# Kernel optimization log

Measured on AMD Instinct MI355X. Metric: run time of the kernel, lower is better.

The kernel has to match this reference:

```python
import jax, jax.numpy as jnp
import numpy as np

MAX_JOINTS = 143

def setup_inputs() -> dict:
    key = jax.random.key(0)
    ks = jax.random.split(key, 8)
    d_model, latent_dim, feat = 256, 512, 13
    s = lambda n: 1.0 / np.sqrt(n)
    return {
        "z": jax.random.normal(ks[0], (32, latent_dim), jnp.float32),
        "W_latent": jax.random.normal(ks[1], (latent_dim, d_model), jnp.float32) * s(latent_dim),
        "b_latent": jnp.zeros((d_model,), jnp.float32),
        "joint_emb": jax.random.normal(ks[2], (MAX_JOINTS, d_model), jnp.float32),
        "frame_emb": jax.random.normal(ks[3], (120, d_model), jnp.float32),
        "ln_gamma": jnp.ones((d_model,), jnp.float32),
        "ln_beta": jnp.zeros((d_model,), jnp.float32),
        "W1": jax.random.normal(ks[4], (d_model, d_model), jnp.float32) * s(d_model),
        "b1": jnp.zeros((d_model,), jnp.float32),
        "W2": jax.random.normal(ks[5], (d_model, feat), jnp.float32) * s(d_model),
        "b2": jnp.zeros((feat,), jnp.float32),
        "max_frames": 120,
    }

def reference(z, W_latent, b_latent, joint_emb, frame_emb, ln_gamma, ln_beta, W1, b1, W2, b2, max_frames):
    # base: [B, d]
    base = z @ W_latent + b_latent
    fe = frame_emb[:max_frames]  # [F, d]
    # three-way broadcast sum -> [B, J, F, d]
    hidden = base[:, None, None, :] + joint_emb[None, :, None, :] + fe[None, None, :, :]
    # LayerNorm over last dim (eps=1e-5, torch default)
    mu = jnp.mean(hidden, axis=-1, keepdims=True)
    var = jnp.mean(jnp.square(hidden - mu), axis=-1, keepdims=True)
    h = (hidden - mu) * jax.lax.rsqrt(var + 1e-5) * ln_gamma + ln_beta
    # MLP: Linear -> exact GELU -> Linear
    h = jax.nn.gelu(h @ W1 + b1, approximate=False)
    out = h @ W2 + b2  # [B, J, F, feat]
    return jnp.transpose(out, (0, 1, 3, 2))  # [B, J, feat, F]
```

## Files before the change

kernel.cpp:

```cpp
#include <hip/hip_runtime.h>
#include <hip/hip_bf16.h>
#include <hip/hip_cooperative_groups.h>

namespace cg = cooperative_groups;

typedef __bf16 bf16x8 __attribute__((ext_vector_type(8)));
typedef float  f32x4  __attribute__((ext_vector_type(4)));
typedef float  f32x2  __attribute__((ext_vector_type(2)));

#define B_  32
#define J_  143
#define F_  120
#define D_  256
#define L_  512
#define C_  13
#define M_  4576
#define MP_ 4736
#define FE0 4576
#define NK  512
#define NN  384
#define GRID_  763
#define PAIRS_ 2288

static __device__ __forceinline__ unsigned short bits(__bf16 h) {
  return __builtin_bit_cast(unsigned short, h);
}

__device__ __forceinline__ f32x2 gelu2(f32x2 u) {
  f32x2 x2 = u * u;
  f32x2 t  = u * (x2 * -0.1029432f + -2.3022082f);
  f32x2 e;
  e.x = __builtin_amdgcn_exp2f(t.x);
  e.y = __builtin_amdgcn_exp2f(t.y);
  f32x2 d = e + 1.0f;
  f32x2 r;
  r.x = __builtin_amdgcn_rcpf(d.x);
  r.y = __builtin_amdgcn_rcpf(d.y);
  return u * r;
}

__global__ __launch_bounds__(256, 3) void fused_kernel(
    int phase,
    const float* __restrict__ z, const float* __restrict__ Wl,
    const float* __restrict__ bl, const float* __restrict__ joint,
    const float* __restrict__ fe, const float* __restrict__ gamma,
    const float* __restrict__ beta, const float* __restrict__ W1,
    const float* __restrict__ b1, const float* __restrict__ W2,
    const float* __restrict__ b2,
    float* __restrict__ base, unsigned short* __restrict__ BT,
    float* __restrict__ bW1, float* __restrict__ Sfe, float* __restrict__ Sfe2,
    unsigned short* __restrict__ W2T, float* __restrict__ zerov,
    float* __restrict__ PX, float* __restrict__ Sc, float* __restrict__ Sc2,
    float* __restrict__ out) {
  __shared__ float zs[L_];
  __shared__ float ra[4], rb[4];
  __shared__ float pc[2][256], bw[256], rstdl[2][128];
  __shared__ __align__(16) unsigned short w2l[4096];

  const int tid  = threadIdx.x;
  const int lane = tid & 63, wv = tid >> 6;
  const int lrow = lane & 15, lgrp = lane >> 4;
  const int bid  = blockIdx.x;
  const bool coop = (phase == 0);

  if (coop || phase == 1) {
    if (bid < 32) {
      zs[tid]       = z[bid * L_ + tid];
      zs[tid + 256] = z[bid * L_ + tid + 256];
      __syncthreads();
      float acc = 0.f;
      #pragma unroll 32
      for (int k = 0; k < L_; ++k) acc = __builtin_fmaf(zs[k], Wl[k * D_ + tid], acc);
      base[bid * D_ + tid] = acc + bl[tid];
    } else if (bid < 433) {
      const int n = bid - 32;
      if (n < 256) {
        const float w1v = W1[tid * D_ + n];
        float a = gamma[tid] * w1v;
        float b = beta[tid] * w1v;
        const float wg = a;
        #pragma unroll
        for (int m = 1; m < 64; m <<= 1) { a += __shfl_xor(a, m); b += __shfl_xor(b, m); }
        if (lane == 0) { ra[wv] = a; rb[wv] = b; }
        __syncthreads();
        const float cs = ra[0] + ra[1] + ra[2] + ra[3];
        if (tid == 0) bW1[n] = rb[0] + rb[1] + rb[2] + rb[3] + b1[n];
        const float m = __builtin_fmaf(cs, -1.f / 256.f, wg);
        const __bf16 hi = (__bf16)m;
        const __bf16 lo = (__bf16)(m - (float)hi);
        BT[n * NK + tid]       = bits(hi);
        BT[n * NK + 256 + tid] = bits(lo);
      } else if (n < 376) {
        const int f = n - 256;
        const float v = fe[f * D_ + tid];
        float a = v, b = v * v;
        #pragma unroll
        for (int m = 1; m < 64; m <<= 1) { a += __shfl_xor(a, m); b += __shfl_xor(b, m); }
        if (lane == 0) { ra[wv] = a; rb[wv] = b; }
        __syncthreads();
        if (tid == 0) {
          Sfe[f]  = ra[0] + ra[1] + ra[2] + ra[3];
          Sfe2[f] = rb[0] + rb[1] + rb[2] + rb[3];
        }
        const __bf16 hi = (__bf16)v;
        const __bf16 lo = (__bf16)(v - (float)hi);
        BT[n * NK + tid]       = bits(hi);
        BT[n * NK + 256 + tid] = bits(lo);
      } else if (n < 384) {
        BT[n * NK + tid] = 0; BT[n * NK + 256 + tid] = 0;
      } else if (n < 400) {
        const int c = n - 384;
        const float v = (c < C_) ? W2[tid * C_ + c] : 0.f;
        W2T[c * D_ + tid] = bits((__bf16)v);
      } else {
        zerov[tid] = 0.f;
      }
    }
  }
  if (coop) cg::this_grid().sync();

  if ((coop || phase == 2) && bid < 444) {
    const int rb_ = bid / 6, cb_ = bid % 6;
    const int rowbase = rb_ * 64 + wv * 16;
    const int colbase = cb_ * 64;
    const int r = rowbase + lrow;

    const float *p1, *p2;
    if (r < M_) {
      const int b = r / J_, j = r - b * J_;
      p1 = base + b * D_; p2 = joint + j * D_;
    } else if (r < FE0 + F_) {
      p1 = fe + (r - FE0) * D_; p2 = zerov;
    } else {
      p1 = zerov; p2 = zerov;
    }

    const unsigned short* Bp = BT + (size_t)(colbase + lrow) * NK + lgrp * 8;
    f32x4 acc[4] = {};
    float ssum = 0.f, ssq = 0.f;
    #pragma unroll
    for (int s8 = 0; s8 < 8; ++s8) {
      const int k0 = s8 * 32 + lgrp * 8;
      const float4 ca = *(const float4*)(p1 + k0);
      const float4 cb4 = *(const float4*)(p1 + k0 + 4);
      const float4 da = *(const float4*)(p2 + k0);
      const float4 db = *(const float4*)(p2 + k0 + 4);
      const float c[8] = {ca.x + da.x, ca.y + da.y, ca.z + da.z, ca.w + da.w,
                          cb4.x + db.x, cb4.y + db.y, cb4.z + db.z, cb4.w + db.w};
      bf16x8 ahi, alo;
      #pragma unroll
      for (int e = 0; e < 8; ++e) {
        const __bf16 h = (__bf16)c[e];
        ahi[e] = h;
        alo[e] = (__bf16)(c[e] - (float)h);
      }
      if (cb_ == 0) {
        #pragma unroll
        for (int e = 0; e < 8; ++e) { ssum += c[e]; ssq = __builtin_fmaf(c[e], c[e], ssq); }
      }
      bf16x8 bhi[4], blo[4];
      #pragma unroll
      for (int nf = 0; nf < 4; ++nf) {
        bhi[nf] = *(const bf16x8*)(Bp + (size_t)nf * 16 * NK + s8 * 32);
        blo[nf] = *(const bf16x8*)(Bp + (size_t)nf * 16 * NK + 256 + s8 * 32);
      }
      #pragma unroll
      for (int nf = 0; nf < 4; ++nf)
        acc[nf] = __builtin_amdgcn_mfma_f32_16x16x32_bf16(ahi, bhi[nf], acc[nf], 0, 0, 0);
      #pragma unroll
      for (int nf = 0; nf < 4; ++nf)
        acc[nf] = __builtin_amdgcn_mfma_f32_16x16x32_bf16(alo, bhi[nf], acc[nf], 0, 0, 0);
      #pragma unroll
      for (int nf = 0; nf < 4; ++nf)
        acc[nf] = __builtin_amdgcn_mfma_f32_16x16x32_bf16(ahi, blo[nf], acc[nf], 0, 0, 0);
    }

    if (cb_ == 0) {
      ssum += __shfl_xor(ssum, 16); ssum += __shfl_xor(ssum, 32);
      ssq  += __shfl_xor(ssq, 16);  ssq  += __shfl_xor(ssq, 32);
      if (lgrp == 0) { Sc[r] = ssum; Sc2[r] = ssq; }
    }

    #pragma unroll
    for (int nf = 0; nf < 4; ++nf)
      #pragma unroll
      for (int r4 = 0; r4 < 4; ++r4)
        PX[(size_t)(rowbase + lgrp * 4 + r4) * NN + colbase + nf * 16 + lrow] = acc[nf][r4];
  }
  if (coop) cg::this_grid().sync();

  if (coop || phase == 3) {
    bw[tid] = bW1[tid];
    {
      const int rr = tid >> 4;
      const int b0 = tid * 32;
      const int sb = b0 ^ ((rr & 7) << 4);
      *(uint4*)((char*)w2l + sb)        = *(const uint4*)((const char*)W2T + b0);
      *(uint4*)((char*)w2l + (sb ^ 16)) = *(const uint4*)((const char*)W2T + b0 + 16);
    }
    const float bias = (lrow < C_) ? b2[lrow] : 0.f;

    const int r0 = wv * 32 + lrow, r1 = r0 + 16;
    const int f0 = r0 < F_ ? r0 : F_ - 1;
    const int f1 = r1 < F_ ? r1 : F_ - 1;
    const float* __restrict__ q0p = PX + (size_t)(FE0 + f0) * NN + lgrp * 8;
    const float* __restrict__ q1p = PX + (size_t)(FE0 + f1) * NN + lgrp * 8;

    for (int pair = bid; pair < PAIRS_; pair += (int)gridDim.x) {
      const int bj0 = pair * 2;
      __syncthreads();

      #pragma unroll
      for (int q = 0; q < 2; ++q) pc[q][tid] = PX[(size_t)(bj0 + q) * NN + tid];
      {
        const int q = tid >> 7;
        const int f = tid & 127;
        const int fc = f < F_ ? f : F_ - 1;
        const float X = PX[(size_t)(bj0 + q) * NN + 256 + fc];
        const float mu = (Sc[bj0 + q] + Sfe[fc]) * (1.f / 256.f);
        const float ms = __builtin_fmaf(2.f, X, Sc2[bj0 + q] + Sfe2[fc]) * (1.f / 256.f);
        rstdl[q][f] = rsqrtf(ms - mu * mu + 1e-5f);
      }
      __syncthreads();

      f32x2 RS0[2], RS1[2];
      #pragma unroll
      for (int q = 0; q < 2; ++q) {
        const float a = rstdl[q][r0], b = rstdl[q][r1];
        RS0[q].x = a; RS0[q].y = a;
        RS1[q].x = b; RS1[q].y = b;
      }

      float4 qa0 = *(const float4*)(q0p), qa1 = *(const float4*)(q0p + 4);
      float4 qb0 = *(const float4*)(q1p), qb1 = *(const float4*)(q1p + 4);

      f32x4 acc[2][2] = {};
      #pragma unroll
      for (int s = 0; s < 8; ++s) {
        const int n0 = s * 32 + lgrp * 8;
        float4 na0, na1, nb0, nb1;
        if (s < 7) {
          na0 = *(const float4*)(q0p + (s + 1) * 32);
          na1 = *(const float4*)(q0p + (s + 1) * 32 + 4);
          nb0 = *(const float4*)(q1p + (s + 1) * 32);
          nb1 = *(const float4*)(q1p + (s + 1) * 32 + 4);
        }
        const bf16x8 w2f = *(const bf16x8*)((const char*)w2l +
            ((lrow * 512 + n0 * 2) ^ ((lrow & 7) << 4)));
        const float q0v[8] = {qa0.x, qa0.y, qa0.z, qa0.w, qa1.x, qa1.y, qa1.z, qa1.w};
        const float q1v[8] = {qb0.x, qb0.y, qb0.z, qb0.w, qb1.x, qb1.y, qb1.z, qb1.w};
        bf16x8 af[2][2];
        #pragma unroll
        for (int ep = 0; ep < 4; ++ep) {
          const int e0 = 2 * ep;
          f32x2 Q0, Q1, BV;
          Q0.x = q0v[e0]; Q0.y = q0v[e0 + 1];
          Q1.x = q1v[e0]; Q1.y = q1v[e0 + 1];
          BV = *(const f32x2*)(&bw[n0 + e0]);
          #pragma unroll
          for (int q = 0; q < 2; ++q) {
            const f32x2 P = *(const f32x2*)(&pc[q][n0 + e0]);
            const f32x2 U0 = __builtin_elementwise_fma(RS0[q], P + Q0, BV);
            const f32x2 U1 = __builtin_elementwise_fma(RS1[q], P + Q1, BV);
            const f32x2 G0 = gelu2(U0);
            const f32x2 G1 = gelu2(U1);
            af[q][0][e0] = (__bf16)G0.x; af[q][0][e0 + 1] = (__bf16)G0.y;
            af[q][1][e0] = (__bf16)G1.x; af[q][1][e0 + 1] = (__bf16)G1.y;
          }
        }
        #pragma unroll
        for (int q = 0; q < 2; ++q) {
          acc[q][0] = __builtin_amdgcn_mfma_f32_16x16x32_bf16(af[q][0], w2f, acc[q][0], 0, 0, 0);
          acc[q][1] = __builtin_amdgcn_mfma_f32_16x16x32_bf16(af[q][1], w2f, acc[q][1], 0, 0, 0);
        }
        qa0 = na0; qa1 = na1; qb0 = nb0; qb1 = nb1;
      }

      if (lrow < C_) {
        #pragma unroll
        for (int q = 0; q < 2; ++q)
          #pragma unroll
          for (int mf = 0; mf < 2; ++mf) {
            const int f = wv * 32 + mf * 16 + lgrp * 4;
            if (f < F_) {
              float4 v;
              v.x = acc[q][mf][0] + bias;
              v.y = acc[q][mf][1] + bias;
              v.z = acc[q][mf][2] + bias;
              v.w = acc[q][mf][3] + bias;
              *(float4*)(out + (size_t)(bj0 + q) * (C_ * F_) + lrow * F_ + f) = v;
            }
          }
      }
    }
  }
}

extern "C" void kernel_launch(void* const* d_in, const int* in_sizes, int n_in,
                              void* d_out, int out_size, void* d_ws, size_t ws_size,
                              hipStream_t stream) {
  const float* z     = (const float*)d_in[0];
  const float* Wl    = (const float*)d_in[1];
  const float* bl    = (const float*)d_in[2];
  const float* joint = (const float*)d_in[3];
  const float* fe    = (const float*)d_in[4];
  const float* gamma = (const float*)d_in[5];
  const float* beta  = (const float*)d_in[6];
  const float* W1    = (const float*)d_in[7];
  const float* b1    = (const float*)d_in[8];
  const float* W2    = (const float*)d_in[9];
  const float* b2    = (const float*)d_in[10];
  float* out = (float*)d_out;

  char* ws = (char*)d_ws;
  float*          base  = (float*)(ws + 0);
  unsigned short* W2T   = (unsigned short*)(ws + 32768);
  float*          bW1   = (float*)(ws + 40960);
  float*          Sfe   = (float*)(ws + 41984);
  float*          Sfe2  = (float*)(ws + 42496);
  float*          Sc    = (float*)(ws + 43008);
  float*          Sc2   = (float*)(ws + 61952);
  float*          zerov = (float*)(ws + 80896);
  unsigned short* BT    = (unsigned short*)(ws + 81920);
  float*          PX    = (float*)(ws + 8388608);

  int phase0 = 0;
  void* args[] = {
    (void*)&phase0,
    (void*)&z, (void*)&Wl, (void*)&bl, (void*)&joint, (void*)&fe,
    (void*)&gamma, (void*)&beta, (void*)&W1, (void*)&b1, (void*)&W2, (void*)&b2,
    (void*)&base, (void*)&BT, (void*)&bW1, (void*)&Sfe, (void*)&Sfe2,
    (void*)&W2T, (void*)&zerov, (void*)&PX, (void*)&Sc, (void*)&Sc2, (void*)&out
  };

  int maxB = 0;
  hipError_t qe = hipOccupancyMaxActiveBlocksPerMultiprocessor(&maxB, fused_kernel, 256, 0);
  const bool coopOK = (qe == hipSuccess) && (maxB >= 3);

  if (coopOK) {
    hipLaunchCooperativeKernel((const void*)fused_kernel, dim3(GRID_), dim3(256),
                               args, 0, stream);
  } else {
    fused_kernel<<<433, 256, 0, stream>>>(1, z, Wl, bl, joint, fe, gamma, beta, W1,
        b1, W2, b2, base, BT, bW1, Sfe, Sfe2, W2T, zerov, PX, Sc, Sc2, out);
    fused_kernel<<<444, 256, 0, stream>>>(2, z, Wl, bl, joint, fe, gamma, beta, W1,
        b1, W2, b2, base, BT, bW1, Sfe, Sfe2, W2T, zerov, PX, Sc, Sc2, out);
    fused_kernel<<<PAIRS_, 256, 0, stream>>>(3, z, Wl, bl, joint, fe, gamma, beta, W1,
        b1, W2, b2, base, BT, bW1, Sfe, Sfe2, W2T, zerov, PX, Sc, Sc2, out);
  }
}
```

Before: 83.86 us.

## Split cooperative fused kernel into three ordinary launches with wider phase-3 blocks

Replaces the single cooperative kernel and its two grid-wide barriers with three separate kernels: prep, the split-bf16 GEMM, and the LayerNorm/GELU/second-GEMM stage. The prep stage now handles W1 column reductions in 4 blocks of 64 columns each instead of 256 single-column blocks. The final stage launches one block per 4 (b,j) rows instead of a persistent grid looping over pairs. This removes grid-sync cost and the occupancy constraint, in exchange for two extra launch boundaries and more per-block setup work in the final stage.

```diff
diff --git a/kernel.cpp b/kernel.cpp
--- a/kernel.cpp
+++ b/kernel.cpp
@@ -1,8 +1,5 @@
 #include <hip/hip_runtime.h>
 #include <hip/hip_bf16.h>
-#include <hip/hip_cooperative_groups.h>
-
-namespace cg = cooperative_groups;
 
 typedef __bf16 bf16x8 __attribute__((ext_vector_type(8)));
 typedef float  f32x4  __attribute__((ext_vector_type(4)));
@@ -19,8 +16,6 @@
 #define FE0 4576
 #define NK  512
 #define NN  384
-#define GRID_  763
-#define PAIRS_ 2288
 
 static __device__ __forceinline__ unsigned short bits(__bf16 h) {
   return __builtin_bit_cast(unsigned short, h);
@@ -39,260 +34,279 @@
   return u * r;
 }
 
-__global__ __launch_bounds__(256, 3) void fused_kernel(
-    int phase,
+__global__ __launch_bounds__(256) void prep_kernel(
     const float* __restrict__ z, const float* __restrict__ Wl,
-    const float* __restrict__ bl, const float* __restrict__ joint,
-    const float* __restrict__ fe, const float* __restrict__ gamma,
-    const float* __restrict__ beta, const float* __restrict__ W1,
-    const float* __restrict__ b1, const float* __restrict__ W2,
-    const float* __restrict__ b2,
+    const float* __restrict__ bl, const float* __restrict__ W1,
+    const float* __restrict__ gamma, const float* __restrict__ beta,
+    const float* __restrict__ b1, const float* __restrict__ fe,
+    const float* __restrict__ W2,
     float* __restrict__ base, unsigned short* __restrict__ BT,
     float* __restrict__ bW1, float* __restrict__ Sfe, float* __restrict__ Sfe2,
-    unsigned short* __restrict__ W2T, float* __restrict__ zerov,
-    float* __restrict__ PX, float* __restrict__ Sc, float* __restrict__ Sc2,
-    float* __restrict__ out) {
+    unsigned short* __restrict__ W2T, float* __restrict__ zerov) {
+  const int t = threadIdx.x, bid = blockIdx.x;
+  const int lane = t & 63, wv = t >> 6;
   __shared__ float zs[L_];
   __shared__ float ra[4], rb[4];
-  __shared__ float pc[2][256], bw[256], rstdl[2][128];
+  __shared__ float gml[256], btl[256];
+  __shared__ float redg[4][64], redb[4][64];
+  __shared__ float csl[64];
+
+  if (bid < 32) {
+    zs[t]       = z[bid * L_ + t];
+    zs[t + 256] = z[bid * L_ + t + 256];
+    __syncthreads();
+    float acc = 0.f;
+    #pragma unroll 32
+    for (int k = 0; k < L_; ++k) acc = __builtin_fmaf(zs[k], Wl[k * D_ + t], acc);
+    base[bid * D_ + t] = acc + bl[t];
+    return;
+  }
+  if (bid < 36) {
+    const int n0 = (bid - 32) * 64;
+    const int c  = t & 63;
+    const int kg = t >> 6;
+    gml[t] = gamma[t];
+    btl[t] = beta[t];
+    __syncthreads();
+    float wg = 0.f, wb = 0.f;
+    #pragma unroll 16
+    for (int kk = 0; kk < 64; ++kk) {
+      const int k = kg * 64 + kk;
+      const float w1v = W1[k * D_ + n0 + c];
+      wg = __builtin_fmaf(gml[k], w1v, wg);
+      wb = __builtin_fmaf(btl[k], w1v, wb);
+    }
+    redg[kg][c] = wg;
+    redb[kg][c] = wb;
+    __syncthreads();
+    if (t < 64) {
+      const float cs = redg[0][t] + redg[1][t] + redg[2][t] + redg[3][t];
+      const float bs = redb[0][t] + redb[1][t] + redb[2][t] + redb[3][t];
+      csl[t] = cs * (1.f / 256.f);
+      bW1[n0 + t] = bs + b1[n0 + t];
+    }
+    __syncthreads();
+    const float csc = csl[c];
+    #pragma unroll 16
+    for (int kk = 0; kk < 64; ++kk) {
+      const int k = kg * 64 + kk;
+      const float w1v = W1[k * D_ + n0 + c];
+      const float m = __builtin_fmaf(gml[k], w1v, -csc);
+      const __bf16 hi = (__bf16)m;
+      const __bf16 lo = (__bf16)(m - (float)hi);
+      BT[(n0 + c) * NK + k]       = bits(hi);
+      BT[(n0 + c) * NK + 256 + k] = bits(lo);
+    }
+    return;
+  }
+  if (bid < 156) {
+    const int f = bid - 36;
+    const float v = fe[f * D_ + t];
+    float a = v, b = v * v;
+    #pragma unroll
+    for (int m = 1; m < 64; m <<= 1) { a += __shfl_xor(a, m); b += __shfl_xor(b, m); }
+    if (lane == 0) { ra[wv] = a; rb[wv] = b; }
+    __syncthreads();
+    if (t == 0) {
+      Sfe[f]  = ra[0] + ra[1] + ra[2] + ra[3];
+      Sfe2[f] = rb[0] + rb[1] + rb[2] + rb[3];
+    }
+    const __bf16 hi = (__bf16)v;
+    const __bf16 lo = (__bf16)(v - (float)hi);
+    BT[(256 + f) * NK + t]       = bits(hi);
+    BT[(256 + f) * NK + 256 + t] = bits(lo);
+    return;
+  }
+  #pragma unroll
+  for (int i = 0; i < 16; ++i)
+    BT[376 * NK + i * 256 + t] = 0;
+  #pragma unroll
+  for (int c = 0; c < 16; ++c) {
+    const float v = (c < C_) ? W2[t * C_ + c] : 0.f;
+    W2T[c * D_ + t] = bits((__bf16)v);
+  }
+  zerov[t] = 0.f;
+}
+
+__global__ __launch_bounds__(256, 4) void gemmB_kernel(
+    const float* __restrict__ base, const float* __restrict__ joint,
+    const float* __restrict__ fe, const float* __restrict__ zerov,
+    const unsigned short* __restrict__ BT,
+    float* __restrict__ PX, float* __restrict__ Sc, float* __restrict__ Sc2) {
+  const int tid = threadIdx.x, lane = tid & 63, wave = tid >> 6;
+  const int lrow = lane & 15, lgrp = lane >> 4;
+  const int rb_ = blockIdx.x / 6, cb_ = blockIdx.x % 6;
+  const int rowbase = rb_ * 64 + wave * 16;
+  const int colbase = cb_ * 64;
+  const int r = rowbase + lrow;
+
+  const float *p1, *p2;
+  if (r < M_) {
+    const int b = r / J_, j = r - b * J_;
+    p1 = base + b * D_; p2 = joint + j * D_;
+  } else if (r < FE0 + F_) {
+    p1 = fe + (r - FE0) * D_; p2 = zerov;
+  } else {
+    p1 = zerov; p2 = zerov;
+  }
+
+  const unsigned short* Bp = BT + (size_t)(colbase + lrow) * NK + lgrp * 8;
+  f32x4 acc[4] = {};
+  float ssum = 0.f, ssq = 0.f;
+  #pragma unroll
+  for (int s8 = 0; s8 < 8; ++s8) {
+    const int k0 = s8 * 32 + lgrp * 8;
+    const float4 ca = *(const float4*)(p1 + k0);
+    const float4 cb4 = *(const float4*)(p1 + k0 + 4);
+    const float4 da = *(const float4*)(p2 + k0);
+    const float4 db = *(const float4*)(p2 + k0 + 4);
+    const float c[8] = {ca.x + da.x, ca.y + da.y, ca.z + da.z, ca.w + da.w,
+                        cb4.x + db.x, cb4.y + db.y, cb4.z + db.z, cb4.w + db.w};
+    bf16x8 ahi, alo;
+    #pragma unroll
+    for (int e = 0; e < 8; ++e) {
+      const __bf16 h = (__bf16)c[e];
+      ahi[e] = h;
+      alo[e] = (__bf16)(c[e] - (float)h);
+    }
+    if (cb_ == 0) {
+      #pragma unroll
+      for (int e = 0; e < 8; ++e) { ssum += c[e]; ssq = __builtin_fmaf(c[e], c[e], ssq); }
+    }
+    bf16x8 bhi[4], blo[4];
+    #pragma unroll
+    for (int nf = 0; nf < 4; ++nf) {
+      bhi[nf] = *(const bf16x8*)(Bp + (size_t)nf * 16 * NK + s8 * 32);
+      blo[nf] = *(const bf16x8*)(Bp + (size_t)nf * 16 * NK + 256 + s8 * 32);
+    }
+    #pragma unroll
+    for (int nf = 0; nf < 4; ++nf)
+      acc[nf] = __builtin_amdgcn_mfma_f32_16x16x32_bf16(ahi, bhi[nf], acc[nf], 0, 0, 0);
+    #pragma unroll
+    for (int nf = 0; nf < 4; ++nf)
+      acc[nf] = __builtin_amdgcn_mfma_f32_16x16x32_bf16(alo, bhi[nf], acc[nf], 0, 0, 0);
+    #pragma unroll
+    for (int nf = 0; nf < 4; ++nf)
+      acc[nf] = __builtin_amdgcn_mfma_f32_16x16x32_bf16(ahi, blo[nf], acc[nf], 0, 0, 0);
+  }
+
+  if (cb_ == 0) {
+    ssum += __shfl_xor(ssum, 16); ssum += __shfl_xor(ssum, 32);
+    ssq  += __shfl_xor(ssq, 16);  ssq  += __shfl_xor(ssq, 32);
+    if (lgrp == 0) { Sc[r] = ssum; Sc2[r] = ssq; }
+  }
+
+  #pragma unroll
+  for (int nf = 0; nf < 4; ++nf)
+    #pragma unroll
+    for (int r4 = 0; r4 < 4; ++r4)
+      PX[(size_t)(rowbase + lgrp * 4 + r4) * NN + colbase + nf * 16 + lrow] = acc[nf][r4];
+}
+
+__global__ __launch_bounds__(256, 4) void mainC_kernel(
+    const float* __restrict__ PX, const float* __restrict__ bW1,
+    const float* __restrict__ Sc, const float* __restrict__ Sc2,
+    const float* __restrict__ Sfe, const float* __restrict__ Sfe2,
+    const unsigned short* __restrict__ W2T, const float* __restrict__ b2,
+    float* __restrict__ out) {
+  __shared__ float pc[4][256], bw[256], rstdl[4][128];
   __shared__ __align__(16) unsigned short w2l[4096];
-
-  const int tid  = threadIdx.x;
-  const int lane = tid & 63, wv = tid >> 6;
+  const int tid = threadIdx.x, lane = tid & 63, wv = tid >> 6;
   const int lrow = lane & 15, lgrp = lane >> 4;
-  const int bid  = blockIdx.x;
-  const bool coop = (phase == 0);
-
-  if (coop || phase == 1) {
-    if (bid < 32) {
-      zs[tid]       = z[bid * L_ + tid];
-      zs[tid + 256] = z[bid * L_ + tid + 256];
-      __syncthreads();
-      float acc = 0.f;
-      #pragma unroll 32
-      for (int k = 0; k < L_; ++k) acc = __builtin_fmaf(zs[k], Wl[k * D_ + tid], acc);
-      base[bid * D_ + tid] = acc + bl[tid];
-    } else if (bid < 433) {
-      const int n = bid - 32;
-      if (n < 256) {
-        const float w1v = W1[tid * D_ + n];
-        float a = gamma[tid] * w1v;
-        float b = beta[tid] * w1v;
-        const float wg = a;
-        #pragma unroll
-        for (int m = 1; m < 64; m <<= 1) { a += __shfl_xor(a, m); b += __shfl_xor(b, m); }
-        if (lane == 0) { ra[wv] = a; rb[wv] = b; }
-        __syncthreads();
-        const float cs = ra[0] + ra[1] + ra[2] + ra[3];
-        if (tid == 0) bW1[n] = rb[0] + rb[1] + rb[2] + rb[3] + b1[n];
-        const float m = __builtin_fmaf(cs, -1.f / 256.f, wg);
-        const __bf16 hi = (__bf16)m;
-        const __bf16 lo = (__bf16)(m - (float)hi);
-        BT[n * NK + tid]       = bits(hi);
-        BT[n * NK + 256 + tid] = bits(lo);
-      } else if (n < 376) {
-        const int f = n - 256;
-        const float v = fe[f * D_ + tid];
-        float a = v, b = v * v;
-        #pragma unroll
-        for (int m = 1; m < 64; m <<= 1) { a += __shfl_xor(a, m); b += __shfl_xor(b, m); }
-        if (lane == 0) { ra[wv] = a; rb[wv] = b; }
-        __syncthreads();
-        if (tid == 0) {
-          Sfe[f]  = ra[0] + ra[1] + ra[2] + ra[3];
-          Sfe2[f] = rb[0] + rb[1] + rb[2] + rb[3];
+  const int bj0 = blockIdx.x * 4;
+
+  #pragma unroll
+  for (int q = 0; q < 4; ++q) pc[q][tid] = PX[(size_t)(bj0 + q) * NN + tid];
+  bw[tid] = bW1[tid];
+  {
+    const int rr = tid >> 4;
+    const int b0 = tid * 32;
+    const int sb = b0 ^ ((rr & 7) << 4);
+    *(uint4*)((char*)w2l + sb)        = *(const uint4*)((const char*)W2T + b0);
+    *(uint4*)((char*)w2l + (sb ^ 16)) = *(const uint4*)((const char*)W2T + b0 + 16);
+  }
+  #pragma unroll
+  for (int qq = 0; qq < 2; ++qq) {
+    const int idx = tid + qq * 256;
+    const int q = idx >> 7;
+    const int f = idx & 127;
+    const int fc = f < F_ ? f : F_ - 1;
+    const float X = PX[(size_t)(bj0 + q) * NN + 256 + fc];
+    const float mu = (Sc[bj0 + q] + Sfe[fc]) * (1.f / 256.f);
+    const float ms = __builtin_fmaf(2.f, X, Sc2[bj0 + q] + Sfe2[fc]) * (1.f / 256.f);
+    rstdl[q][f] = rsqrtf(ms - mu * mu + 1e-5f);
+  }
+  __syncthreads();
+
+  const int r0 = wv * 32 + lrow, r1 = r0 + 16;
+  const int f0 = r0 < F_ ? r0 : F_ - 1;
+  const int f1 = r1 < F_ ? r1 : F_ - 1;
+  float rs0[4], rs1[4];
+  #pragma unroll
+  for (int q = 0; q < 4; ++q) { rs0[q] = rstdl[q][r0]; rs1[q] = rstdl[q][r1]; }
+  const float* __restrict__ q0p = PX + (size_t)(FE0 + f0) * NN + lgrp * 8;
+  const float* __restrict__ q1p = PX + (size_t)(FE0 + f1) * NN + lgrp * 8;
+
+  float4 qa0 = *(const float4*)(q0p), qa1 = *(const float4*)(q0p + 4);
+  float4 qb0 = *(const float4*)(q1p), qb1 = *(const float4*)(q1p + 4);
+
+  f32x4 acc[4][2] = {};
+  #pragma unroll
+  for (int s = 0; s < 8; ++s) {
+    const int n0 = s * 32 + lgrp * 8;
+    float4 na0, na1, nb0, nb1;
+    if (s < 7) {
+      na0 = *(const float4*)(q0p + (s + 1) * 32);
+      na1 = *(const float4*)(q0p + (s + 1) * 32 + 4);
+      nb0 = *(const float4*)(q1p + (s + 1) * 32);
+      nb1 = *(const float4*)(q1p + (s + 1) * 32 + 4);
+    }
+    const bf16x8 w2f = *(const bf16x8*)((const char*)w2l +
+        ((lrow * 512 + n0 * 2) ^ ((lrow & 7) << 4)));
+    const float q0v[8] = {qa0.x, qa0.y, qa0.z, qa0.w, qa1.x, qa1.y, qa1.z, qa1.w};
+    const float q1v[8] = {qb0.x, qb0.y, qb0.z, qb0.w, qb1.x, qb1.y, qb1.z, qb1.w};
+    #pragma unroll
+    for (int q = 0; q < 4; ++q) {
+      bf16x8 af0, af1;
+      #pragma unroll
+      for (int ep = 0; ep < 4; ++ep) {
+        const int e0 = 2 * ep;
+        f32x2 Q0, Q1, BV;
+        Q0.x = q0v[e0]; Q0.y = q0v[e0 + 1];
+        Q1.x = q1v[e0]; Q1.y = q1v[e0 + 1];
+        BV = *(const f32x2*)(&bw[n0 + e0]);
+        const f32x2 P = *(const f32x2*)(&pc[q][n0 + e0]);
+        f32x2 RS0; RS0.x = rs0[q]; RS0.y = rs0[q];
+        f32x2 RS1; RS1.x = rs1[q]; RS1.y = rs1[q];
+        const f32x2 U0 = __builtin_elementwise_fma(RS0, P + Q0, BV);
+        const f32x2 U1 = __builtin_elementwise_fma(RS1, P + Q1, BV);
+        const f32x2 G0 = gelu2(U0);
+        const f32x2 G1 = gelu2(U1);
+        af0[e0] = (__bf16)G0.x; af0[e0 + 1] = (__bf16)G0.y;
+        af1[e0] = (__bf16)G1.x; af1[e0 + 1] = (__bf16)G1.y;
+      }
+      acc[q][0] = __builtin_amdgcn_mfma_f32_16x16x32_bf16(af0, w2f, acc[q][0], 0, 0, 0);
+      acc[q][1] = __builtin_amdgcn_mfma_f32_16x16x32_bf16(af1, w2f, acc[q][1], 0, 0, 0);
+    }
+    qa0 = na0; qa1 = na1; qb0 = nb0; qb1 = nb1;
+  }
+
+  if (lrow < C_) {
+    const float bias = b2[lrow];
+    #pragma unroll
+    for (int q = 0; q < 4; ++q)
+      #pragma unroll
+      for (int mf = 0; mf < 2; ++mf) {
+        const int f = wv * 32 + mf * 16 + lgrp * 4;
+        if (f < F_) {
+          float4 v;
+          v.x = acc[q][mf][0] + bias;
+          v.y = acc[q][mf][1] + bias;
+          v.z = acc[q][mf][2] + bias;
+          v.w = acc[q][mf][3] + bias;
+          *(float4*)(out + (size_t)(bj0 + q) * (C_ * F_) + lrow * F_ + f) = v;
         }
-        const __bf16 hi = (__bf16)v;
-        const __bf16 lo = (__bf16)(v - (float)hi);
-        BT[n * NK + tid]       = bits(hi);
-        BT[n * NK + 256 + tid] = bits(lo);
-      } else if (n < 384) {
-        BT[n * NK + tid] = 0; BT[n * NK + 256 + tid] = 0;
-      } else if (n < 400) {
-        const int c = n - 384;
-        const float v = (c < C_) ? W2[tid * C_ + c] : 0.f;
-        W2T[c * D_ + tid] = bits((__bf16)v);
-      } else {
-        zerov[tid] = 0.f;
       }
-    }
-  }
-  if (coop) cg::this_grid().sync();
-
-  if ((coop || phase == 2) && bid < 444) {
-    const int rb_ = bid / 6, cb_ = bid % 6;
-    const int rowbase = rb_ * 64 + wv * 16;
-    const int colbase = cb_ * 64;
-    const int r = rowbase + lrow;
-
-    const float *p1, *p2;
-    if (r < M_) {
-      const int b = r / J_, j = r - b * J_;
-      p1 = base + b * D_; p2 = joint + j * D_;
-    } else if (r < FE0 + F_) {
-      p1 = fe + (r - FE0) * D_; p2 = zerov;
-    } else {
-      p1 = zerov; p2 = zerov;
-    }
-
-    const unsigned short* Bp = BT + (size_t)(colbase + lrow) * NK + lgrp * 8;
-    f32x4 acc[4] = {};
-    float ssum = 0.f, ssq = 0.f;
-    #pragma unroll
-    for (int s8 = 0; s8 < 8; ++s8) {
-      const int k0 = s8 * 32 + lgrp * 8;
-      const float4 ca = *(const float4*)(p1 + k0);
-      const float4 cb4 = *(const float4*)(p1 + k0 + 4);
-      const float4 da = *(const float4*)(p2 + k0);
-      const float4 db = *(const float4*)(p2 + k0 + 4);
-      const float c[8] = {ca.x + da.x, ca.y + da.y, ca.z + da.z, ca.w + da.w,
-                          cb4.x + db.x, cb4.y + db.y, cb4.z + db.z, cb4.w + db.w};
-      bf16x8 ahi, alo;
-      #pragma unroll
-      for (int e = 0; e < 8; ++e) {
-        const __bf16 h = (__bf16)c[e];
-        ahi[e] = h;
-        alo[e] = (__bf16)(c[e] - (float)h);
-      }
-      if (cb_ == 0) {
-        #pragma unroll
-        for (int e = 0; e < 8; ++e) { ssum += c[e]; ssq = __builtin_fmaf(c[e], c[e], ssq); }
-      }
-      bf16x8 bhi[4], blo[4];
-      #pragma unroll
-      for (int nf = 0; nf < 4; ++nf) {
-        bhi[nf] = *(const bf16x8*)(Bp + (size_t)nf * 16 * NK + s8 * 32);
-        blo[nf] = *(const bf16x8*)(Bp + (size_t)nf * 16 * NK + 256 + s8 * 32);
-      }
-      #pragma unroll
-      for (int nf = 0; nf < 4; ++nf)
-        acc[nf] = __builtin_amdgcn_mfma_f32_16x16x32_bf16(ahi, bhi[nf], acc[nf], 0, 0, 0);
-      #pragma unroll
-      for (int nf = 0; nf < 4; ++nf)
-        acc[nf] = __builtin_amdgcn_mfma_f32_16x16x32_bf16(alo, bhi[nf], acc[nf], 0, 0, 0);
-      #pragma unroll
-      for (int nf = 0; nf < 4; ++nf)
-        acc[nf] = __builtin_amdgcn_mfma_f32_16x16x32_bf16(ahi, blo[nf], acc[nf], 0, 0, 0);
-    }
-
-    if (cb_ == 0) {
-      ssum += __shfl_xor(ssum, 16); ssum += __shfl_xor(ssum, 32);
-      ssq  += __shfl_xor(ssq, 16);  ssq  += __shfl_xor(ssq, 32);
-      if (lgrp == 0) { Sc[r] = ssum; Sc2[r] = ssq; }
-    }
-
-    #pragma unroll
-    for (int nf = 0; nf < 4; ++nf)
-      #pragma unroll
-      for (int r4 = 0; r4 < 4; ++r4)
-        PX[(size_t)(rowbase + lgrp * 4 + r4) * NN + colbase + nf * 16 + lrow] = acc[nf][r4];
-  }
-  if (coop) cg::this_grid().sync();
-
-  if (coop || phase == 3) {
-    bw[tid] = bW1[tid];
-    {
-      const int rr = tid >> 4;
-      const int b0 = tid * 32;
-      const int sb = b0 ^ ((rr & 7) << 4);
-      *(uint4*)((char*)w2l + sb)        = *(const uint4*)((const char*)W2T + b0);
-      *(uint4*)((char*)w2l + (sb ^ 16)) = *(const uint4*)((const char*)W2T + b0 + 16);
-    }
-    const float bias = (lrow < C_) ? b2[lrow] : 0.f;
-
-    const int r0 = wv * 32 + lrow, r1 = r0 + 16;
-    const int f0 = r0 < F_ ? r0 : F_ - 1;
-    const int f1 = r1 < F_ ? r1 : F_ - 1;
-    const float* __restrict__ q0p = PX + (size_t)(FE0 + f0) * NN + lgrp * 8;
-    const float* __restrict__ q1p = PX + (size_t)(FE0 + f1) * NN + lgrp * 8;
-
-    for (int pair = bid; pair < PAIRS_; pair += (int)gridDim.x) {
-      const int bj0 = pair * 2;
-      __syncthreads();
-
-      #pragma unroll
-      for (int q = 0; q < 2; ++q) pc[q][tid] = PX[(size_t)(bj0 + q) * NN + tid];
-      {
-        const int q = tid >> 7;
-        const int f = tid & 127;
-        const int fc = f < F_ ? f : F_ - 1;
-        const float X = PX[(size_t)(bj0 + q) * NN + 256 + fc];
-        const float mu = (Sc[bj0 + q] + Sfe[fc]) * (1.f / 256.f);
-        const float ms = __builtin_fmaf(2.f, X, Sc2[bj0 + q] + Sfe2[fc]) * (1.f / 256.f);
-        rstdl[q][f] = rsqrtf(ms - mu * mu + 1e-5f);
-      }
-      __syncthreads();
-
-      f32x2 RS0[2], RS1[2];
-      #pragma unroll
-      for (int q = 0; q < 2; ++q) {
-        const float a = rstdl[q][r0], b = rstdl[q][r1];
-        RS0[q].x = a; RS0[q].y = a;
-        RS1[q].x = b; RS1[q].y = b;
-      }
-
-      float4 qa0 = *(const float4*)(q0p), qa1 = *(const float4*)(q0p + 4);
-      float4 qb0 = *(const float4*)(q1p), qb1 = *(const float4*)(q1p + 4);
-
-      f32x4 acc[2][2] = {};
-      #pragma unroll
-      for (int s = 0; s < 8; ++s) {
-        const int n0 = s * 32 + lgrp * 8;
-        float4 na0, na1, nb0, nb1;
-        if (s < 7) {
-          na0 = *(const float4*)(q0p + (s + 1) * 32);
-          na1 = *(const float4*)(q0p + (s + 1) * 32 + 4);
-          nb0 = *(const float4*)(q1p + (s + 1) * 32);
-          nb1 = *(const float4*)(q1p + (s + 1) * 32 + 4);
-        }
-        const bf16x8 w2f = *(const bf16x8*)((const char*)w2l +
-            ((lrow * 512 + n0 * 2) ^ ((lrow & 7) << 4)));
-        const float q0v[8] = {qa0.x, qa0.y, qa0.z, qa0.w, qa1.x, qa1.y, qa1.z, qa1.w};
-        const float q1v[8] = {qb0.x, qb0.y, qb0.z, qb0.w, qb1.x, qb1.y, qb1.z, qb1.w};
-        bf16x8 af[2][2];
-        #pragma unroll
-        for (int ep = 0; ep < 4; ++ep) {
-          const int e0 = 2 * ep;
-          f32x2 Q0, Q1, BV;
-          Q0.x = q0v[e0]; Q0.y = q0v[e0 + 1];
-          Q1.x = q1v[e0]; Q1.y = q1v[e0 + 1];
-          BV = *(const f32x2*)(&bw[n0 + e0]);
-          #pragma unroll
-          for (int q = 0; q < 2; ++q) {
-            const f32x2 P = *(const f32x2*)(&pc[q][n0 + e0]);
-            const f32x2 U0 = __builtin_elementwise_fma(RS0[q], P + Q0, BV);
-            const f32x2 U1 = __builtin_elementwise_fma(RS1[q], P + Q1, BV);
-            const f32x2 G0 = gelu2(U0);
-            const f32x2 G1 = gelu2(U1);
-            af[q][0][e0] = (__bf16)G0.x; af[q][0][e0 + 1] = (__bf16)G0.y;
-            af[q][1][e0] = (__bf16)G1.x; af[q][1][e0 + 1] = (__bf16)G1.y;
-          }
-        }
-        #pragma unroll
-        for (int q = 0; q < 2; ++q) {
-          acc[q][0] = __builtin_amdgcn_mfma_f32_16x16x32_bf16(af[q][0], w2f, acc[q][0], 0, 0, 0);
-          acc[q][1] = __builtin_amdgcn_mfma_f32_16x16x32_bf16(af[q][1], w2f, acc[q][1], 0, 0, 0);
-        }
-        qa0 = na0; qa1 = na1; qb0 = nb0; qb1 = nb1;
-      }
-
-      if (lrow < C_) {
-        #pragma unroll
-        for (int q = 0; q < 2; ++q)
-          #pragma unroll
-          for (int mf = 0; mf < 2; ++mf) {
-            const int f = wv * 32 + mf * 16 + lgrp * 4;
-            if (f < F_) {
-              float4 v;
-              v.x = acc[q][mf][0] + bias;
-              v.y = acc[q][mf][1] + bias;
-              v.z = acc[q][mf][2] + bias;
-              v.w = acc[q][mf][3] + bias;
-              *(float4*)(out + (size_t)(bj0 + q) * (C_ * F_) + lrow * F_ + f) = v;
-            }
-          }
-      }
-    }
   }
 }
 
@@ -324,28 +338,8 @@
   unsigned short* BT    = (unsigned short*)(ws + 81920);
   float*          PX    = (float*)(ws + 8388608);
 
-  int phase0 = 0;
-  void* args[] = {
-    (void*)&phase0,
-    (void*)&z, (void*)&Wl, (void*)&bl, (void*)&joint, (void*)&fe,
-    (void*)&gamma, (void*)&beta, (void*)&W1, (void*)&b1, (void*)&W2, (void*)&b2,
-    (void*)&base, (void*)&BT, (void*)&bW1, (void*)&Sfe, (void*)&Sfe2,
-    (void*)&W2T, (void*)&zerov, (void*)&PX, (void*)&Sc, (void*)&Sc2, (void*)&out
-  };
-
-  int maxB = 0;
-  hipError_t qe = hipOccupancyMaxActiveBlocksPerMultiprocessor(&maxB, fused_kernel, 256, 0);
-  const bool coopOK = (qe == hipSuccess) && (maxB >= 3);
-
-  if (coopOK) {
-    hipLaunchCooperativeKernel((const void*)fused_kernel, dim3(GRID_), dim3(256),
-                               args, 0, stream);
-  } else {
-    fused_kernel<<<433, 256, 0, stream>>>(1, z, Wl, bl, joint, fe, gamma, beta, W1,
-        b1, W2, b2, base, BT, bW1, Sfe, Sfe2, W2T, zerov, PX, Sc, Sc2, out);
-    fused_kernel<<<444, 256, 0, stream>>>(2, z, Wl, bl, joint, fe, gamma, beta, W1,
-        b1, W2, b2, base, BT, bW1, Sfe, Sfe2, W2T, zerov, PX, Sc, Sc2, out);
-    fused_kernel<<<PAIRS_, 256, 0, stream>>>(3, z, Wl, bl, joint, fe, gamma, beta, W1,
-        b1, W2, b2, base, BT, bW1, Sfe, Sfe2, W2T, zerov, PX, Sc, Sc2, out);
-  }
-}
+  prep_kernel<<<157, 256, 0, stream>>>(z, Wl, bl, W1, gamma, beta, b1, fe, W2,
+                                       base, BT, bW1, Sfe, Sfe2, W2T, zerov);
+  gemmB_kernel<<<444, 256, 0, stream>>>(base, joint, fe, zerov, BT, PX, Sc, Sc2);
+  mainC_kernel<<<M_ / 4, 256, 0, stream>>>(PX, bW1, Sc, Sc2, Sfe, Sfe2, W2T, b2, out);
+}
```

New measurement: 95.47 us. 1.14x slower.
